# Performance work log

Measured on AMD Instinct MI355X. Metric: run time of the kernel, lower is better.

The kernel has to match this reference:

```python
import jax, jax.numpy as jnp
import jax.scipy.fft as jsp_fft
import numpy as np

B, NX, NY, DV = 4, 512, 512, 32
KX, KY = 64, 64


def setup_inputs() -> dict:
    key = jax.random.key(0)
    k1, k2, k3 = jax.random.split(key, 3)
    x = jax.random.normal(k1, (B, NX, NY, DV), dtype=jnp.float32)
    R_real = jax.random.uniform(k2, (DV, DV, KX, KY), dtype=jnp.float32)
    R_imag = jax.random.uniform(k3, (DV, DV, KX, KY), dtype=jnp.float32)
    return {"x": x, "R_real": R_real, "R_imag": R_imag}


def reference(x, R_real, R_imag):
    # x: [B, nX, nY, dv]
    R = R_real + 1j * R_imag  # [dv_out, dv_in, kX, kY]
    kX, kY = R.shape[-2:]
    nX = x.shape[1]

    xt = jnp.moveaxis(x, -1, -3)                      # [B, dv, nX, nY]
    xd = jsp_fft.dct(xt, type=2, axis=-1, norm='ortho')   # DCT-II along Y
    xf = jnp.fft.rfft(xd, axis=-2, norm='ortho')      # [B, dv, nX//2+1, nY] complex
    nXf, nY = xf.shape[-2:]

    # Truncation einsum with identity-padded T matrices == slicing
    xtr = xf[..., :kX, :kY]                           # [B, dv, kX, kY]
    # Per-mode complex channel mixing
    y = jnp.einsum('ijab,ejab->eiab', R, xtr)         # [B, dv, kX, kY]
    # Inverse truncation == zero-padding back to full spectrum
    yp = jnp.pad(y, ((0, 0), (0, 0), (0, nXf - kX), (0, nY - kY)))

    yr = jnp.fft.irfft(yp, n=nX, axis=-2, norm='ortho')
    yd = jsp_fft.idct(yr, type=2, axis=-1, norm='ortho')
    return jnp.moveaxis(yd, -3, -1)                   # [B, nX, nY, dv]
```

## Files before the change

kernel.cpp:

```cpp
#include <hip/hip_runtime.h>
#include <math.h>

#define BB 4
#define NXD 512
#define NYD 512
#define DVD 32
#define KXD 64
#define KYD 64

#define OFF_DN  0
#define OFF_DT  32768
#define OFF_FCN 65536
#define OFF_FSN 98304
#define OFF_FI2 131072
#define OFF_C   196608
#define OFF_FR  4390912
#define OFF_FI  4915200
#define OFF_YR  5439488
#define OFF_YI  5963776
#define OFF_G   6488064

__device__ __forceinline__ void gload_lds16(const float* g, float* l) {
    __builtin_amdgcn_global_load_lds(
        (const __attribute__((address_space(1))) void*)g,
        (__attribute__((address_space(3))) void*)l, 16, 0, 0);
}

__global__ __launch_bounds__(256) void k_tables(float* __restrict__ ws) {
    int idx = blockIdx.x * 256 + threadIdx.x;
    int k = idx >> 9;
    int n = idx & 511;
    const float inv_sq512 = 0.04419417382415922f;
    float ak = (k == 0) ? inv_sq512 : 0.0625f;
    int m = (k * (2 * n + 1)) & 2047;
    float d = ak * cospif((float)m * (1.0f / 1024.0f));
    ws[OFF_DN + k * 512 + n] = d;
    ws[OFF_DT + n * 64 + k] = d;
    int mf = (k * n) & 511;
    float c = cospif((float)mf * (1.0f / 256.0f)) * inv_sq512;
    float s = sinpif((float)mf * (1.0f / 256.0f)) * inv_sq512;
    ws[OFF_FCN + k * 512 + n] = c;
    ws[OFF_FSN + k * 512 + n] = s;
    ws[OFF_FI2 + (n * 64 + k) * 2 + 0] = c;
    ws[OFF_FI2 + (n * 64 + k) * 2 + 1] = s;
}

__global__ __launch_bounds__(256) void k_dct(const float* __restrict__ x,
                                             const float* __restrict__ ws,
                                             float* __restrict__ C) {
    __shared__ __align__(16) float xs[2][2][1024];
    __shared__ __align__(16) float dt[2][2048];
    int b = blockIdx.x >> 8;
    int nx = (blockIdx.x & 255) * 2;
    int t = threadIdx.x;
    int wv = t >> 6;
    int dv0 = (t & 15) * 2;
    int ky0 = (t >> 4) * 4;
    const float* Dt = ws + OFF_DT;
    const float* xb = x + (size_t)(b * NXD + nx) * NYD * DVD;

    auto stage = [&](int buf, int ch) {
#pragma unroll
        for (int n = 0; n < 2; ++n)
            gload_lds16(xb + (size_t)(n * 512 + ch * 32) * 32 + t * 4,
                        &xs[buf][n][wv * 256]);
#pragma unroll
        for (int p = 0; p < 2; ++p)
            gload_lds16(Dt + ch * 2048 + (p * 256 + t) * 4,
                        &dt[buf][(p * 256 + wv * 64) * 4]);
    };

    float a[2][4][2] = {};
    stage(0, 0);
    __syncthreads();
    for (int ch = 0; ch < 16; ++ch) {
        int buf = ch & 1;
        if (ch < 15) stage(buf ^ 1, ch + 1);
        const float* dtc = &dt[buf][ky0];
        const float* x0p = &xs[buf][0][dv0];
        const float* x1p = &xs[buf][1][dv0];
#pragma unroll 4
        for (int nyc = 0; nyc < 32; ++nyc) {
            float4 d4 = *(const float4*)(dtc + nyc * 64);
            float2 x0 = *(const float2*)(x0p + nyc * 32);
            float2 x1 = *(const float2*)(x1p + nyc * 32);
            float da[4] = {d4.x, d4.y, d4.z, d4.w};
#pragma unroll
            for (int q = 0; q < 4; ++q) {
                a[0][q][0] += da[q] * x0.x; a[0][q][1] += da[q] * x0.y;
                a[1][q][0] += da[q] * x1.x; a[1][q][1] += da[q] * x1.y;
            }
        }
        __syncthreads();
    }
#pragma unroll
    for (int n = 0; n < 2; ++n)
#pragma unroll
        for (int q = 0; q < 4; ++q) {
            float2 v; v.x = a[n][q][0]; v.y = a[n][q][1];
            *(float2*)(C + ((size_t)((b * KYD + ky0 + q) * NXD + nx + n)) * DVD + dv0) = v;
        }
}

__global__ __launch_bounds__(256) void k_rfft(const float* __restrict__ Cbuf,
                                              const float* __restrict__ ws,
                                              float* __restrict__ Fr,
                                              float* __restrict__ Fi) {
    __shared__ __align__(16) float cs[256 * 16];
    int b = blockIdx.x >> 7;
    int r = blockIdx.x & 127;
    int ky = r >> 1;
    int dvbase = (r & 1) * 16;
    int t = threadIdx.x;
    int dv0 = (t & 7) * 2;
    int kx0 = (t >> 3) * 2;
    const float* T2 = ws + OFF_FI2;
    float ar[2][2] = {}, ai[2][2] = {};
    for (int ch = 0; ch < 2; ++ch) {
        int nx0 = ch * 256;
        __syncthreads();
#pragma unroll
        for (int p = 0; p < 4; ++p) {
            int fi4 = p * 256 + t;
            int row = fi4 >> 2, c4 = fi4 & 3;
            *(float4*)(cs + row * 16 + c4 * 4) =
                *(const float4*)(Cbuf + ((size_t)(b * KYD + ky) * NXD + nx0 + row) * DVD + dvbase + c4 * 4);
        }
        __syncthreads();
#pragma unroll 8
        for (int nxc = 0; nxc < 256; ++nxc) {
            float2 cv = *(const float2*)(cs + nxc * 16 + dv0);
            float4 q = *(const float4*)(T2 + ((nx0 + nxc) * 64 + kx0) * 2);
            ar[0][0] += q.x * cv.x; ar[0][1] += q.x * cv.y;
            ai[0][0] -= q.y * cv.x; ai[0][1] -= q.y * cv.y;
            ar[1][0] += q.z * cv.x; ar[1][1] += q.z * cv.y;
            ai[1][0] -= q.w * cv.x; ai[1][1] -= q.w * cv.y;
        }
    }
#pragma unroll
    for (int q = 0; q < 2; ++q) {
        size_t o = ((size_t)((b * KYD + ky) * KXD + kx0 + q)) * DVD + dvbase + dv0;
        float2 vr; vr.x = ar[q][0]; vr.y = ar[q][1];
        float2 vi; vi.x = ai[q][0]; vi.y = ai[q][1];
        *(float2*)(Fr + o) = vr;
        *(float2*)(Fi + o) = vi;
    }
}

__global__ __launch_bounds__(256) void k_mix(const float* __restrict__ Rr,
                                             const float* __restrict__ Ri,
                                             const float* __restrict__ Fr,
                                             const float* __restrict__ Fi,
                                             float* __restrict__ Yr,
                                             float* __restrict__ Yi) {
    __shared__ float fl[2 * 32 * 64 * 2];
    int kx = blockIdx.x & 63;
    int ig = (blockIdx.x >> 6) & 7;
    int eh = blockIdx.x >> 9;
    int t = threadIdx.x;
    int j = t & 31, kyb = t >> 5;
#pragma unroll
    for (int e2 = 0; e2 < 2; ++e2) {
        int e = eh * 2 + e2;
#pragma unroll
        for (int p = 0; p < 8; ++p) {
            int ky = p * 8 + kyb;
            size_t go = ((size_t)((e * KYD + ky) * KXD + kx)) * DVD + j;
            int lo = ((e2 * 32 + j) * 64 + ((ky + j) & 63)) * 2;
            fl[lo] = Fr[go];
            fl[lo + 1] = Fi[go];
        }
    }
    __syncthreads();
    int lane = t & 63, w = t >> 6;
    int i = ig * 4 + w;
    size_t rb = (size_t)(i * 32) * 4096 + kx * 64 + lane;
    float yr[2] = {}, yi[2] = {};
#pragma unroll 8
    for (int jj = 0; jj < 32; ++jj) {
        float rr = Rr[rb + (size_t)jj * 4096];
        float ri = Ri[rb + (size_t)jj * 4096];
#pragma unroll
        for (int e2 = 0; e2 < 2; ++e2) {
            float2 f = *(const float2*)(fl + ((e2 * 32 + jj) * 64 + ((lane + jj) & 63)) * 2);
            yr[e2] += rr * f.x - ri * f.y;
            yi[e2] += rr * f.y + ri * f.x;
        }
    }
#pragma unroll
    for (int e2 = 0; e2 < 2; ++e2) {
        int e = eh * 2 + e2;
        size_t o = ((size_t)((e * DVD + i) * KXD + kx)) * KYD + lane;
        Yr[o] = yr[e2];
        Yi[o] = yi[e2];
    }
}

__global__ __launch_bounds__(256) void k_irfft(const float* __restrict__ Yr,
                                               const float* __restrict__ Yi,
                                               const float* __restrict__ ws,
                                               float* __restrict__ G) {
    __shared__ __align__(16) float ylr[64 * 64];
    __shared__ __align__(16) float yli[64 * 64];
    int blk = blockIdx.x;
    int oct = blk & 7;
    int i = (blk >> 3) & 31;
    int b = blk >> 8;
    int t = threadIdx.x;
    size_t ybase = ((size_t)(b * DVD + i)) * KXD * KYD;
#pragma unroll
    for (int p = 0; p < 4; ++p) {
        int f = p * 256 + t;
        float wk = (f < 16) ? 1.0f : 2.0f;
        float4 vr = *(const float4*)(Yr + ybase + (size_t)f * 4);
        float4 vi = *(const float4*)(Yi + ybase + (size_t)f * 4);
        vr.x *= wk; vr.y *= wk; vr.z *= wk; vr.w *= wk;
        vi.x *= wk; vi.y *= wk; vi.z *= wk; vi.w *= wk;
        *(float4*)(ylr + f * 4) = vr;
        *(float4*)(yli + f * 4) = vi;
    }
    __syncthreads();
    int kyg = t & 15, nxg = t >> 4;
    int ky0 = kyg * 4;
    int gnx0 = oct * 64 + nxg * 4;
    const float* Tc = ws + OFF_FCN;
    const float* Ts = ws + OFF_FSN;
    float acc[4][4] = {};
    for (int kx = 0; kx < 64; ++kx) {
        float4 cv = *(const float4*)(Tc + kx * 512 + gnx0);
        float4 sv = *(const float4*)(Ts + kx * 512 + gnx0);
        float4 vr = *(const float4*)(ylr + kx * 64 + ky0);
        float4 vi = *(const float4*)(yli + kx * 64 + ky0);
        float ca[4] = {cv.x, cv.y, cv.z, cv.w};
        float sa[4] = {sv.x, sv.y, sv.z, sv.w};
        float ra[4] = {vr.x, vr.y, vr.z, vr.w};
        float ia[4] = {vi.x, vi.y, vi.z, vi.w};
#pragma unroll
        for (int q = 0; q < 4; ++q)
#pragma unroll
            for (int kk = 0; kk < 4; ++kk)
                acc[q][kk] += ca[q] * ra[kk] - sa[q] * ia[kk];
    }
#pragma unroll
    for (int q = 0; q < 4; ++q) {
        float4 v; v.x = acc[q][0]; v.y = acc[q][1]; v.z = acc[q][2]; v.w = acc[q][3];
        *(float4*)(G + (((size_t)(b * NXD + gnx0 + q)) * DVD + i) * KYD + ky0) = v;
    }
}

#define GST 68
__global__ __launch_bounds__(256) void k_idct(const float* __restrict__ G,
                                              const float* __restrict__ ws,
                                              float* __restrict__ out) {
    __shared__ __align__(16) float gs[2][32 * GST];
    __shared__ __align__(16) float dn[2][4096];
    int b = blockIdx.x >> 8;
    int nx = (blockIdx.x & 255) * 2;
    int t = threadIdx.x;
    int wv = t >> 6;
    int ig = t & 15, nyg = t >> 4;
    int i0 = ig * 2;
    const float* Dn = ws + OFF_DN;

    auto stage_dn = [&](int buf, int ch) {
#pragma unroll
        for (int p = 0; p < 4; ++p) {
            int f = p * 256 + t;
            int ky = f >> 4, ny4 = (f & 15) * 4;
            gload_lds16(Dn + ky * 512 + ch * 64 + ny4,
                        &dn[buf][(p * 256 + wv * 64) * 4]);
        }
    };

#pragma unroll
    for (int n = 0; n < 2; ++n) {
        const float4* src = (const float4*)(G + (size_t)(b * NXD + nx + n) * DVD * KYD);
#pragma unroll
        for (int p = 0; p < 2; ++p) {
            int f = p * 256 + t;
            int i = f >> 4, ky4 = (f & 15) * 4;
            *(float4*)(gs[n] + i * GST + ky4) = src[f];
        }
    }
    stage_dn(0, 0);
    __syncthreads();
    float* outb = out + ((size_t)(b * NXD + nx)) * NYD * DVD;
    for (int c = 0; c < 8; ++c) {
        int buf = c & 1;
        if (c < 7) stage_dn(buf ^ 1, c + 1);
        float acc[2][4][2] = {};
#pragma unroll 2
        for (int kyc = 0; kyc < 16; ++kyc) {
            int ky0 = kyc * 4;
            float4 g00 = *(const float4*)(gs[0] + i0 * GST + ky0);
            float4 g01 = *(const float4*)(gs[0] + (i0 + 1) * GST + ky0);
            float4 g10 = *(const float4*)(gs[1] + i0 * GST + ky0);
            float4 g11 = *(const float4*)(gs[1] + (i0 + 1) * GST + ky0);
            float g0a[2][4] = {{g00.x, g00.y, g00.z, g00.w}, {g10.x, g10.y, g10.z, g10.w}};
            float g1a[2][4] = {{g01.x, g01.y, g01.z, g01.w}, {g11.x, g11.y, g11.z, g11.w}};
#pragma unroll
            for (int kk = 0; kk < 4; ++kk) {
                float4 dv = *(const float4*)(&dn[buf][(ky0 + kk) * 64 + nyg * 4]);
                float da[4] = {dv.x, dv.y, dv.z, dv.w};
#pragma unroll
                for (int q = 0; q < 4; ++q) {
                    acc[0][q][0] += da[q] * g0a[0][kk];
                    acc[0][q][1] += da[q] * g1a[0][kk];
                    acc[1][q][0] += da[q] * g0a[1][kk];
                    acc[1][q][1] += da[q] * g1a[1][kk];
                }
            }
        }
        int ny0 = c * 64 + nyg * 4;
#pragma unroll
        for (int n = 0; n < 2; ++n)
#pragma unroll
            for (int q = 0; q < 4; ++q) {
                float2 v; v.x = acc[n][q][0]; v.y = acc[n][q][1];
                *(float2*)(outb + ((size_t)n * NYD + ny0 + q) * DVD + i0) = v;
            }
        __syncthreads();
    }
}

extern "C" void kernel_launch(void* const* d_in, const int* in_sizes, int n_in,
                              void* d_out, int out_size, void* d_ws, size_t ws_size,
                              hipStream_t stream) {
    const float* x  = (const float*)d_in[0];
    const float* Rr = (const float*)d_in[1];
    const float* Ri = (const float*)d_in[2];
    float* out = (float*)d_out;
    float* ws  = (float*)d_ws;
    float* C   = ws + OFF_C;
    float* Fr  = ws + OFF_FR;
    float* Fi  = ws + OFF_FI;
    float* Yr  = ws + OFF_YR;
    float* Yi  = ws + OFF_YI;
    float* G   = ws + OFF_G;

    k_tables<<<128, 256, 0, stream>>>(ws);
    k_dct<<<BB * (NXD / 2), 256, 0, stream>>>(x, ws, C);
    k_rfft<<<BB * KYD * 2, 256, 0, stream>>>(C, ws, Fr, Fi);
    k_mix<<<KXD * 8 * 2, 256, 0, stream>>>(Rr, Ri, Fr, Fi, Yr, Yi);
    k_irfft<<<BB * DVD * 8, 256, 0, stream>>>(Yr, Yi, ws, G);
    k_idct<<<BB * NXD / 2, 256, 0, stream>>>(G, ws, out);
}
```

Measured before the change: 405.7 us.

## Enlarge per-thread register tiles in DCT and IDCT kernels, swizzle LDS

The DCT kernel now runs 128-thread blocks in which each thread computes a 4x4x2 output tile instead of 4x2x2, which raises arithmetic intensity per LDS load and allows float4 stores. The IDCT kernel doubles each thread's channel tile to 4, replaces padded G storage with an XOR-swizzled layout to avoid bank conflicts, and stages 128-column Dn chunks single-buffered with explicit syncs instead of double-buffering. This cuts LDS traffic per FMA and the number of loop iterations, in exchange for more register pressure, fewer threads per block in the DCT, and less load/compute overlap in the IDCT.

New measurement: 404.4 us. About the same (-0.3%).

```diff
diff --git a/kernel.cpp b/kernel.cpp
--- a/kernel.cpp
+++ b/kernel.cpp
@@ -45,7 +45,7 @@
     ws[OFF_FI2 + (n * 64 + k) * 2 + 1] = s;
 }
 
-__global__ __launch_bounds__(256) void k_dct(const float* __restrict__ x,
+__global__ __launch_bounds__(128) void k_dct(const float* __restrict__ x,
                                              const float* __restrict__ ws,
                                              float* __restrict__ C) {
     __shared__ __align__(16) float xs[2][2][1024];
@@ -54,23 +54,25 @@
     int nx = (blockIdx.x & 255) * 2;
     int t = threadIdx.x;
     int wv = t >> 6;
-    int dv0 = (t & 15) * 2;
-    int ky0 = (t >> 4) * 4;
+    int dv0 = (t & 7) * 4;
+    int ky0 = (t >> 3) * 4;
     const float* Dt = ws + OFF_DT;
     const float* xb = x + (size_t)(b * NXD + nx) * NYD * DVD;
 
     auto stage = [&](int buf, int ch) {
 #pragma unroll
         for (int n = 0; n < 2; ++n)
-            gload_lds16(xb + (size_t)(n * 512 + ch * 32) * 32 + t * 4,
-                        &xs[buf][n][wv * 256]);
-#pragma unroll
-        for (int p = 0; p < 2; ++p)
-            gload_lds16(Dt + ch * 2048 + (p * 256 + t) * 4,
-                        &dt[buf][(p * 256 + wv * 64) * 4]);
+#pragma unroll
+            for (int p = 0; p < 2; ++p)
+                gload_lds16(xb + (size_t)(n * 512 + ch * 32) * 32 + (p * 128 + t) * 4,
+                            &xs[buf][n][(p * 128 + wv * 64) * 4]);
+#pragma unroll
+        for (int p = 0; p < 4; ++p)
+            gload_lds16(Dt + ch * 2048 + (p * 128 + t) * 4,
+                        &dt[buf][(p * 128 + wv * 64) * 4]);
     };
 
-    float a[2][4][2] = {};
+    float acc[2][4][4] = {};
     stage(0, 0);
     __syncthreads();
     for (int ch = 0; ch < 16; ++ch) {
@@ -82,14 +84,17 @@
 #pragma unroll 4
         for (int nyc = 0; nyc < 32; ++nyc) {
             float4 d4 = *(const float4*)(dtc + nyc * 64);
-            float2 x0 = *(const float2*)(x0p + nyc * 32);
-            float2 x1 = *(const float2*)(x1p + nyc * 32);
+            float4 x0 = *(const float4*)(x0p + nyc * 32);
+            float4 x1 = *(const float4*)(x1p + nyc * 32);
             float da[4] = {d4.x, d4.y, d4.z, d4.w};
-#pragma unroll
-            for (int q = 0; q < 4; ++q) {
-                a[0][q][0] += da[q] * x0.x; a[0][q][1] += da[q] * x0.y;
-                a[1][q][0] += da[q] * x1.x; a[1][q][1] += da[q] * x1.y;
-            }
+            float xa[2][4] = {{x0.x, x0.y, x0.z, x0.w}, {x1.x, x1.y, x1.z, x1.w}};
+#pragma unroll
+            for (int q = 0; q < 4; ++q)
+#pragma unroll
+                for (int d = 0; d < 4; ++d) {
+                    acc[0][q][d] += da[q] * xa[0][d];
+                    acc[1][q][d] += da[q] * xa[1][d];
+                }
         }
         __syncthreads();
     }
@@ -97,8 +102,9 @@
     for (int n = 0; n < 2; ++n)
 #pragma unroll
         for (int q = 0; q < 4; ++q) {
-            float2 v; v.x = a[n][q][0]; v.y = a[n][q][1];
-            *(float2*)(C + ((size_t)((b * KYD + ky0 + q) * NXD + nx + n)) * DVD + dv0) = v;
+            float4 v; v.x = acc[n][q][0]; v.y = acc[n][q][1];
+            v.z = acc[n][q][2]; v.w = acc[n][q][3];
+            *(float4*)(C + ((size_t)((b * KYD + ky0 + q) * NXD + nx + n)) * DVD + dv0) = v;
         }
 }
 
@@ -248,27 +254,26 @@
     }
 }
 
-#define GST 68
 __global__ __launch_bounds__(256) void k_idct(const float* __restrict__ G,
                                               const float* __restrict__ ws,
                                               float* __restrict__ out) {
-    __shared__ __align__(16) float gs[2][32 * GST];
-    __shared__ __align__(16) float dn[2][4096];
+    __shared__ __align__(16) float gs[2][2048];
+    __shared__ __align__(16) float dn[8192];
     int b = blockIdx.x >> 8;
     int nx = (blockIdx.x & 255) * 2;
     int t = threadIdx.x;
     int wv = t >> 6;
-    int ig = t & 15, nyg = t >> 4;
-    int i0 = ig * 2;
+    int ig = t & 7;
+    int nyg = t >> 3;
+    int i0 = ig * 4;
     const float* Dn = ws + OFF_DN;
 
-    auto stage_dn = [&](int buf, int ch) {
-#pragma unroll
-        for (int p = 0; p < 4; ++p) {
+    auto stage_dn = [&](int c) {
+#pragma unroll
+        for (int p = 0; p < 8; ++p) {
             int f = p * 256 + t;
-            int ky = f >> 4, ny4 = (f & 15) * 4;
-            gload_lds16(Dn + ky * 512 + ch * 64 + ny4,
-                        &dn[buf][(p * 256 + wv * 64) * 4]);
+            int ky = f >> 5, ny4 = (f & 31) * 4;
+            gload_lds16(Dn + ky * 512 + c * 128 + ny4, dn + (p * 256 + wv * 64) * 4);
         }
     };
 
@@ -278,48 +283,54 @@
 #pragma unroll
         for (int p = 0; p < 2; ++p) {
             int f = p * 256 + t;
-            int i = f >> 4, ky4 = (f & 15) * 4;
-            *(float4*)(gs[n] + i * GST + ky4) = src[f];
-        }
-    }
-    stage_dn(0, 0);
+            int i = f >> 4, c4 = f & 15;
+            int c4s = (c4 ^ (i >> 2)) & 15;
+            *(float4*)(gs[n] + i * 64 + c4s * 4) = src[f];
+        }
+    }
+    stage_dn(0);
     __syncthreads();
     float* outb = out + ((size_t)(b * NXD + nx)) * NYD * DVD;
-    for (int c = 0; c < 8; ++c) {
-        int buf = c & 1;
-        if (c < 7) stage_dn(buf ^ 1, c + 1);
-        float acc[2][4][2] = {};
+    for (int c = 0; c < 4; ++c) {
+        float acc[2][4][4] = {};
 #pragma unroll 2
         for (int kyc = 0; kyc < 16; ++kyc) {
             int ky0 = kyc * 4;
-            float4 g00 = *(const float4*)(gs[0] + i0 * GST + ky0);
-            float4 g01 = *(const float4*)(gs[0] + (i0 + 1) * GST + ky0);
-            float4 g10 = *(const float4*)(gs[1] + i0 * GST + ky0);
-            float4 g11 = *(const float4*)(gs[1] + (i0 + 1) * GST + ky0);
-            float g0a[2][4] = {{g00.x, g00.y, g00.z, g00.w}, {g10.x, g10.y, g10.z, g10.w}};
-            float g1a[2][4] = {{g01.x, g01.y, g01.z, g01.w}, {g11.x, g11.y, g11.z, g11.w}};
+            float ga[2][4][4];
+#pragma unroll
+            for (int n = 0; n < 2; ++n)
+#pragma unroll
+                for (int di = 0; di < 4; ++di) {
+                    float4 g = *(const float4*)(gs[n] + (i0 + di) * 64 + ((kyc ^ ig) & 15) * 4);
+                    ga[n][di][0] = g.x; ga[n][di][1] = g.y;
+                    ga[n][di][2] = g.z; ga[n][di][3] = g.w;
+                }
 #pragma unroll
             for (int kk = 0; kk < 4; ++kk) {
-                float4 dv = *(const float4*)(&dn[buf][(ky0 + kk) * 64 + nyg * 4]);
-                float da[4] = {dv.x, dv.y, dv.z, dv.w};
-#pragma unroll
-                for (int q = 0; q < 4; ++q) {
-                    acc[0][q][0] += da[q] * g0a[0][kk];
-                    acc[0][q][1] += da[q] * g1a[0][kk];
-                    acc[1][q][0] += da[q] * g0a[1][kk];
-                    acc[1][q][1] += da[q] * g1a[1][kk];
-                }
+                float4 dv4 = *(const float4*)(dn + (ky0 + kk) * 128 + nyg * 4);
+                float dq[4] = {dv4.x, dv4.y, dv4.z, dv4.w};
+#pragma unroll
+                for (int q = 0; q < 4; ++q)
+#pragma unroll
+                    for (int n = 0; n < 2; ++n)
+#pragma unroll
+                        for (int di = 0; di < 4; ++di)
+                            acc[n][q][di] += dq[q] * ga[n][di][kk];
             }
         }
-        int ny0 = c * 64 + nyg * 4;
 #pragma unroll
         for (int n = 0; n < 2; ++n)
 #pragma unroll
             for (int q = 0; q < 4; ++q) {
-                float2 v; v.x = acc[n][q][0]; v.y = acc[n][q][1];
-                *(float2*)(outb + ((size_t)n * NYD + ny0 + q) * DVD + i0) = v;
+                float4 v; v.x = acc[n][q][0]; v.y = acc[n][q][1];
+                v.z = acc[n][q][2]; v.w = acc[n][q][3];
+                *(float4*)(outb + ((size_t)(n * NYD + c * 128 + nyg * 4 + q)) * DVD + i0) = v;
             }
-        __syncthreads();
+        if (c < 3) {
+            __syncthreads();
+            stage_dn(c + 1);
+            __syncthreads();
+        }
     }
 }
 
@@ -339,7 +350,7 @@
     float* G   = ws + OFF_G;
 
     k_tables<<<128, 256, 0, stream>>>(ws);
-    k_dct<<<BB * (NXD / 2), 256, 0, stream>>>(x, ws, C);
+    k_dct<<<BB * (NXD / 2), 128, 0, stream>>>(x, ws, C);
     k_rfft<<<BB * KYD * 2, 256, 0, stream>>>(C, ws, Fr, Fi);
     k_mix<<<KXD * 8 * 2, 256, 0, stream>>>(Rr, Ri, Fr, Fi, Yr, Yi);
     k_irfft<<<BB * DVD * 8, 256, 0, stream>>>(Yr, Yi, ws, G);
```
